# Performance work log

Hardware: AMD Instinct MI355X
Metric: run time of the kernel (lower is better)

The kernel has to match this reference:

```python
import jax, jax.numpy as jnp
import numpy as np

NUM_NODES = 100000
NUM_EDGES = 1600000
NUM_GRAPHS = 1000
NUM_REP = 16
R_DIM = 16
N_SCALARS = 16
N_CLASSES = 6
N_LAYERS = 3
L_MAX = 1
EPS = 1e-8


def get_rot(v):
    """2x2 SO(2) rotation from 2D vector angle, L_max=1. v:[n,2] -> [n,1,2,2]."""
    theta = jnp.arctan2(v[:, 1], v[:, 0])
    c, s = jnp.cos(theta), jnp.sin(theta)
    R = jnp.stack([jnp.stack([c, -s], -1), jnp.stack([s, c], -1)], -2)  # [n,2,2]
    return R[:, None]  # [n, L_max=1, 2, 2]


def bessel(d, number=R_DIM, end=1.0):
    """Bessel radial basis sqrt(2/end)*sin(n*pi*d/end)/d. d:[E] -> [E,number]."""
    n = jnp.arange(1, number + 1, dtype=d.dtype)
    d_safe = d[:, None] + EPS
    return jnp.sqrt(2.0 / end) * jnp.sin(n * jnp.pi * d[:, None] / end) / d_safe


def seg_sum(x, idx, n):
    return jax.ops.segment_sum(x, idx, num_segments=n)


def setup_inputs() -> dict:
    key = jax.random.key(0)
    ks = jax.random.split(key, 20)
    pos = jax.random.normal(ks[0], (NUM_NODES, 2), dtype=jnp.float32)
    edge_index = jax.random.randint(ks[1], (2, NUM_EDGES), 0, NUM_NODES)
    batch = jnp.sort(jax.random.randint(ks[2], (NUM_NODES,), 0, NUM_GRAPHS))
    s = 0.1
    return {
        "pos": pos,
        "W_emb_rot": s * jax.random.normal(ks[3], (NUM_REP, L_MAX, 2), jnp.float32),
        "w_s_emb": s * jax.random.normal(ks[4], (N_SCALARS,), jnp.float32),
        "b_s_emb": jnp.zeros((N_SCALARS,), jnp.float32),
        "Wg": s * jax.random.normal(ks[5], (N_LAYERS, R_DIM, NUM_REP), jnp.float32),
        "bg": jnp.zeros((N_LAYERS, NUM_REP), jnp.float32),
        "Wmix": s * jax.random.normal(ks[6], (N_LAYERS, NUM_REP, NUM_REP), jnp.float32),
        "Wgate": s * jax.random.normal(ks[7], (N_LAYERS, N_SCALARS, NUM_REP), jnp.float32),
        "bgate": jnp.zeros((N_LAYERS, NUM_REP), jnp.float32),
        "Ws1": s * jax.random.normal(ks[8], (N_LAYERS, N_SCALARS + R_DIM, N_SCALARS), jnp.float32),
        "bs1": jnp.zeros((N_LAYERS, N_SCALARS), jnp.float32),
        "W1": s * jax.random.normal(ks[9], (N_SCALARS + NUM_REP * L_MAX * 2, 3 * (N_SCALARS + NUM_REP * L_MAX * 2)), jnp.float32),
        "b1": jnp.zeros((3 * (N_SCALARS + NUM_REP * L_MAX * 2),), jnp.float32),
        "W2": s * jax.random.normal(ks[10], (3 * (N_SCALARS + NUM_REP * L_MAX * 2), N_CLASSES), jnp.float32),
        "b2": jnp.zeros((N_CLASSES,), jnp.float32),
        "edge_index": edge_index,
        "batch": batch,
    }


def reference(pos, W_emb_rot, w_s_emb, b_s_emb, Wg, bg, Wmix, Wgate, bgate,
              Ws1, bs1, W1, b1, W2, b2, edge_index, batch):
    N = pos.shape[0]
    # --- geometry under no_grad in torch ---
    posg = jax.lax.stop_gradient(pos)
    cnt = seg_sum(jnp.ones((N,), posg.dtype), batch, NUM_GRAPHS)
    mean = seg_sum(posg, batch, NUM_GRAPHS) / jnp.maximum(cnt, 1.0)[:, None]
    posg = posg - mean[batch]
    rot_theta = get_rot(posg)                        # [N,1,2,2]
    row, col = edge_index[0], edge_index[1]
    edge_vec = posg[row] - posg[col]                 # [E,2]
    rot = get_rot(edge_vec)                          # [E,1,2,2]
    dist = jnp.linalg.norm(edge_vec, axis=1)         # [E]

    dist_emb = bessel(dist)                          # [E,r_dim]

    # --- edge embedding -> node features ---
    e_rot = jnp.einsum('eklm,jkm->ejkl', rot, W_emb_rot)      # [E,rep,1,2]
    deg = jnp.maximum(seg_sum(jnp.ones((row.shape[0],), pos.dtype), row, N), 1.0)
    x_rot = seg_sum(e_rot, row, N) / deg[:, None, None, None]  # [N,rep,1,2]
    d_mean = seg_sum(dist, row, N) / deg
    x_s = jax.nn.leaky_relu(d_mean[:, None] * w_s_emb[None, :] + b_s_emb)  # [N,ns]

    rot_inv = jnp.swapaxes(rot, -1, -2)
    # --- EqBlocks: gather -> rotate-in -> radial mix -> rotate-out -> scatter ---
    for i in range(N_LAYERS):
        local = jnp.einsum('eklm,ejkm->ejkl', rot_inv, x_rot[col])   # [E,rep,1,2]
        g = dist_emb @ Wg[i] + bg[i]                                 # [E,rep]
        local = jnp.einsum('ij,ejkl->eikl', Wmix[i], local) * g[:, :, None, None]
        msg = jnp.einsum('eklm,ejkm->ejkl', rot, local)              # [E,rep,1,2]
        agg = seg_sum(msg, row, N) / deg[:, None, None, None]
        gate = jax.nn.sigmoid(x_s @ Wgate[i] + bgate[i])             # [N,rep]
        x_rot = x_rot + agg * gate[:, :, None, None]
        msg_s = jax.nn.leaky_relu(
            jnp.concatenate([x_s[col], dist_emb], axis=1) @ Ws1[i] + bs1[i])
        x_s = x_s + seg_sum(msg_s, row, N) / deg[:, None]

    # --- SO2OutU (faithful to given source) ---
    rot_theta_inv = jnp.swapaxes(rot_theta, -1, -2)                  # [N,1,2,2]
    x_out = jnp.einsum('njkm,nkml->njkl', x_rot, rot_theta_inv)      # [N,rep,1,2]
    x_cat = jnp.concatenate([x_s, x_out.reshape(N, -1)], axis=1)    # [N,48]
    u = jax.nn.leaky_relu(x_cat @ W1 + b1) @ W2 + b2                 # [N,n_classes]
    return seg_sum(u, batch, NUM_GRAPHS)                             # [G,n_classes]
```

## Files before the change

### kernel.cpp

```cpp
#include <hip/hip_runtime.h>
#include <hip/hip_fp16.h>
#include <math.h>

#define NREP 16
#define RDIM 16
#define NS   16
#define NC   6
#define H1   144
#define DBINS 64
#define TILE 4096
#define NBMAX 512
#define P2CAP 10240

static __device__ __forceinline__ float leaky(float v) { return v > 0.0f ? v : 0.01f * v; }

__global__ void __launch_bounds__(256) k_gsum_bhist(
    const float* __restrict__ pos, const int* __restrict__ batch, int N,
    float* __restrict__ gsum, float* __restrict__ gcnt,
    const int* __restrict__ ei, int E, int* __restrict__ bhist) {
  int t = threadIdx.x;
  __shared__ int h[NBMAX];
  for (int i = t; i < NBMAX; i += 256) h[i] = 0;
  __syncthreads();
  int base = blockIdx.x * TILE;
  int lim = min(base + TILE, E);
  for (int j = base + t; j < lim; j += 256) atomicAdd(&h[ei[j] >> 8], 1);
  __syncthreads();
  for (int i = t; i < NBMAX; i += 256)
    if (h[i] > 0) atomicAdd(&bhist[i], h[i]);

  __shared__ float bx[320], by[320], bc[320];
  int start = blockIdx.x * 256;
  if (start >= N) return;
  int n = start + t;
  int b0 = batch[min(start, N - 1)];
  int span = batch[min(start + 255, N - 1)] - b0;
  bool useLds = (span < 320);
  if (useLds) {
    for (int i = t; i <= span; i += 256) { bx[i] = 0.f; by[i] = 0.f; bc[i] = 0.f; }
    __syncthreads();
    if (n < N) {
      int rb = batch[n] - b0;
      atomicAdd(&bx[rb], pos[2 * n + 0]);
      atomicAdd(&by[rb], pos[2 * n + 1]);
      atomicAdd(&bc[rb], 1.0f);
    }
    __syncthreads();
    for (int i = t; i <= span; i += 256) {
      if (bc[i] != 0.0f) {
        atomicAdd(&gsum[2 * (b0 + i) + 0], bx[i]);
        atomicAdd(&gsum[2 * (b0 + i) + 1], by[i]);
        atomicAdd(&gcnt[b0 + i], bc[i]);
      }
    }
  } else if (n < N) {
    int b = batch[n];
    atomicAdd(&gsum[2 * b + 0], pos[2 * n + 0]);
    atomicAdd(&gsum[2 * b + 1], pos[2 * n + 1]);
    atomicAdd(&gcnt[b], 1.0f);
  }
}

__global__ void __launch_bounds__(256) k_center_bscan(
    const float* __restrict__ pos, const int* __restrict__ batch, int N, int E,
    const float* __restrict__ gsum, const float* __restrict__ gcnt,
    float* __restrict__ posc, float* __restrict__ cthn, float* __restrict__ sthn,
    const int* __restrict__ bhist, int* __restrict__ bbase, int* __restrict__ bcur, int NB) {
  int t = threadIdx.x;
  if (blockIdx.x == 0) {
    __shared__ int s[NBMAX];
    int v0 = (t < NB) ? bhist[t] : 0;
    int v1 = (t + 256 < NB) ? bhist[t + 256] : 0;
    s[t] = v0; s[t + 256] = v1;
    __syncthreads();
    for (int o = 1; o < NBMAX; o <<= 1) {
      int a0 = (t >= o) ? s[t - o] : 0;
      int a1 = s[t + 256 - o];
      __syncthreads();
      s[t] += a0; s[t + 256] += a1;
      __syncthreads();
    }
    if (t < NB)       { int ex = s[t] - v0;       bbase[t] = ex;       bcur[t] = ex; }
    if (t + 256 < NB) { int ex = s[t + 256] - v1; bbase[t + 256] = ex; bcur[t + 256] = ex; }
    if (t == 0) bbase[NB] = E;
  }
  int i = blockIdx.x * 256 + t;
  if (i < N) {
    int b = batch[i];
    float invc = 1.0f / fmaxf(gcnt[b], 1.0f);
    float px = pos[2 * i + 0] - gsum[2 * b + 0] * invc;
    float py = pos[2 * i + 1] - gsum[2 * b + 1] * invc;
    posc[2 * i + 0] = px;
    posc[2 * i + 1] = py;
    float r = sqrtf(px * px + py * py);
    if (r > 0.0f) { cthn[i] = px / r; sthn[i] = py / r; }
    else          { cthn[i] = 1.0f;  sthn[i] = 0.0f; }
  }
}

__global__ void __launch_bounds__(256) k_part1(
    const int* __restrict__ ei, int E,
    int* __restrict__ bcur, long long* __restrict__ ebuf) {
  __shared__ int hist[NBMAX], lofs[NBMAX], gbase[NBMAX], pc[NBMAX];
  __shared__ long long stg[TILE];
  __shared__ unsigned short bkt[TILE];
  int t = threadIdx.x;
  int base = blockIdx.x * TILE;
  int cntt = min(TILE, E - base);
  for (int i = t; i < NBMAX; i += 256) { hist[i] = 0; pc[i] = 0; }
  __syncthreads();
  int r[16], c[16];
#pragma unroll
  for (int i = 0; i < 16; i++) {
    int e = base + t + i * 256;
    r[i] = -1;
    if (e < E) {
      r[i] = ei[e];
      c[i] = ei[E + e];
      atomicAdd(&hist[r[i] >> 8], 1);
    }
  }
  __syncthreads();
  lofs[t] = hist[t]; lofs[t + 256] = hist[t + 256];
  __syncthreads();
  for (int o = 1; o < NBMAX; o <<= 1) {
    int a0 = (t >= o) ? lofs[t - o] : 0;
    int a1 = lofs[t + 256 - o];
    __syncthreads();
    lofs[t] += a0; lofs[t + 256] += a1;
    __syncthreads();
  }
  int e0 = lofs[t] - hist[t], e1 = lofs[t + 256] - hist[t + 256];
  __syncthreads();
  lofs[t] = e0; lofs[t + 256] = e1;
  __syncthreads();
  for (int i = t; i < NBMAX; i += 256)
    if (hist[i] > 0) gbase[i] = atomicAdd(&bcur[i], hist[i]);
  __syncthreads();
#pragma unroll
  for (int i = 0; i < 16; i++) {
    if (r[i] >= 0) {
      int b = r[i] >> 8;
      int l = lofs[b] + atomicAdd(&pc[b], 1);
      stg[l] = ((long long)r[i] << 32) | (unsigned int)c[i];
      bkt[l] = (unsigned short)b;
    }
  }
  __syncthreads();
  for (int j = t; j < cntt; j += 256) {
    int b = bkt[j];
    ebuf[gbase[b] + (j - lofs[b])] = stg[j];
  }
}

__global__ void __launch_bounds__(256) k_part2(
    const int* __restrict__ bbase, int N, int E,
    const long long* __restrict__ ebuf,
    int* __restrict__ off, int* __restrict__ cnt, int* __restrict__ dhist,
    int* __restrict__ adj) {
  __shared__ int lcnt[256], loff[256], lcur[256];
  __shared__ int lh[DBINS];
  __shared__ int ladj[P2CAP];
  int t = threadIdx.x;
  int b = blockIdx.x;
  int r0 = b << 8;
  int abeg = bbase[b];
  int aend = bbase[b + 1];
  int sz = aend - abeg;
  bool haveRow = (r0 + t < N);
  lcnt[t] = 0;
  if (t < DBINS) lh[t] = 0;
  __syncthreads();
  for (int j = abeg + t; j < aend; j += 256)
    atomicAdd(&lcnt[(int)(ebuf[j] >> 32) - r0], 1);
  __syncthreads();
  int v = lcnt[t];
  loff[t] = v;
  __syncthreads();
  for (int o = 1; o < 256; o <<= 1) {
    int u = (t >= o) ? loff[t - o] : 0;
    __syncthreads();
    loff[t] += u;
    __syncthreads();
  }
  int myoff = loff[t] - v;
  __syncthreads();
  loff[t] = myoff;
  lcur[t] = myoff;
  if (haveRow) {
    off[r0 + t] = abeg + myoff;
    cnt[r0 + t] = v;
    atomicAdd(&lh[min(v, DBINS - 1)], 1);
  }
  if (t == 0 && r0 + 256 >= N) off[N] = E;
  __syncthreads();
  if (t < DBINS && lh[t] > 0) atomicAdd(&dhist[t], lh[t]);
  if (sz <= P2CAP) {
    for (int j = abeg + t; j < aend; j += 256) {
      long long p = ebuf[j];
      int cl = (int)(unsigned int)(p & 0xffffffffLL);
      int rr = (int)(p >> 32) - r0;
      ladj[atomicAdd(&lcur[rr], 1)] = cl;
    }
    __syncthreads();
    for (int j = t; j < sz; j += 256) adj[abeg + j] = ladj[j];
  } else {
    for (int j = abeg + t; j < aend; j += 256) {
      long long p = ebuf[j];
      int cl = (int)(unsigned int)(p & 0xffffffffLL);
      int rr = (int)(p >> 32) - r0;
      adj[abeg + atomicAdd(&lcur[rr], 1)] = cl;
    }
  }
}

__global__ void __launch_bounds__(256) k_init16(
    int N, const int* __restrict__ off, const int* __restrict__ adj,
    const float* __restrict__ posc, float2* __restrict__ spc,
    const float* __restrict__ Wer, const float* __restrict__ wse, const float* __restrict__ bse,
    const float* __restrict__ Wmix, const float* __restrict__ Ws1, const float* __restrict__ bs1,
    const float* __restrict__ Wgate, const float* __restrict__ bgate,
    const int* __restrict__ cnt, const int* __restrict__ dhist,
    int* __restrict__ dcur, int* __restrict__ perm,
    float* __restrict__ xr, float* __restrict__ xs, uint2* __restrict__ yzg) {
  int t = threadIdx.x;
  int nchunk = (N + 255) >> 8;
  if ((int)blockIdx.x < nchunk) {
    __shared__ int sd[DBINS], lh[DBINS], base[DBINS];
    int dv = 0;
    if (t < DBINS) { dv = dhist[t]; sd[t] = dv; lh[t] = 0; }
    __syncthreads();
    for (int o = 1; o < DBINS; o <<= 1) {
      int u = (t >= o && t < DBINS) ? sd[t - o] : 0;
      __syncthreads();
      if (t < DBINS) sd[t] += u;
      __syncthreads();
    }
    int i = blockIdx.x * 256 + t;
    int b = 0, lr = 0;
    if (i < N) {
      b = min(cnt[i], DBINS - 1);
      lr = atomicAdd(&lh[b], 1);
    }
    __syncthreads();
    if (t < DBINS && lh[t] > 0) base[t] = (sd[t] - dv) + atomicAdd(&dcur[t], lh[t]);
    __syncthreads();
    if (i < N) perm[base[b] + lr] = i;
  }

  int idx = blockIdx.x * 256 + t;
  int n = idx >> 4, r = idx & 15;
  if (n >= N) return;
  int a = off[n], b = off[n + 1];
  float px = posc[2 * n + 0], py = posc[2 * n + 1];
  float C = 0.f, S = 0.f, D = 0.f;
  for (int k = a + r; k < b; k += 16) {
    int cl = adj[k];
    float dx = px - posc[2 * cl + 0];
    float dy = py - posc[2 * cl + 1];
    float d = sqrtf(dx * dx + dy * dy);
    float sp, cp;
    sincospif(d, &sp, &cp);
    float spp = 1.41421356237309515f * sp / (d + 1e-8f);
    spc[k] = make_float2(spp, 2.0f * cp);
    if (d > 0.0f) {
      float inv = 1.0f / d;
      C += dx * inv;
      S += dy * inv;
    } else {
      C += 1.0f;
    }
    D += d;
  }
#pragma unroll
  for (int o = 1; o < 16; o <<= 1) {
    C += __shfl_xor(C, o, 16);
    S += __shfl_xor(S, o, 16);
    D += __shfl_xor(D, o, 16);
  }
  float id = 1.0f / fmaxf((float)(b - a), 1.0f);
  C *= id; S *= id;
  float dm = D * id;
  float w0 = Wer[2 * r], w1 = Wer[2 * r + 1];
  float2 x;
  x.x = C * w0 - S * w1;
  x.y = S * w0 + C * w1;
  ((float2*)xr)[(size_t)n * 16 + r] = x;
  float s_new = leaky(dm * wse[r] + bse[r]);
  xs[(size_t)n * 16 + r] = s_new;

  float wmxn[16], wsan[16], wgtn[16];
#pragma unroll
  for (int q = 0; q < 16; q++) wmxn[q] = Wmix[r * 16 + q];
#pragma unroll
  for (int q = 0; q < 16; q++) wsan[q] = Ws1[q * 16 + r];
#pragma unroll
  for (int q = 0; q < 16; q++) wgtn[q] = Wgate[q * 16 + r];
  float y0 = 0.f, y1 = 0.f;
  float z = bs1[r], gtn = bgate[r];
#pragma unroll
  for (int j = 0; j < 16; j++) {
    float xj0 = __shfl(x.x, j, 16);
    float xj1 = __shfl(x.y, j, 16);
    float sj  = __shfl(s_new, j, 16);
    y0 += wmxn[j] * xj0;
    y1 += wmxn[j] * xj1;
    z  += wsan[j] * sj;
    gtn += wgtn[j] * sj;
  }
  gtn = 1.0f / (1.0f + __expf(-gtn));
  __half2 hA = __floats2half2_rn(y0, y1);
  __half2 hB = __floats2half2_rn(z, gtn);
  uint2 w2;
  w2.x = *(unsigned int*)&hA;
  w2.y = *(unsigned int*)&hB;
  yzg[(size_t)n * 16 + r] = w2;
}

__global__ void __launch_bounds__(256) k_layer(
    int N, const int* __restrict__ off,
    const int* __restrict__ adj, const float2* __restrict__ spc,
    const uint2* __restrict__ yzg, const int* __restrict__ perm,
    const float* __restrict__ Wg, const float* __restrict__ bg,
    const float* __restrict__ Ws1,
    float* xr, float* xs,
    int write_next, uint2* __restrict__ yzg_out,
    const float* __restrict__ Wmixn, const float* __restrict__ Ws1n,
    const float* __restrict__ bs1n,
    const float* __restrict__ Wgaten, const float* __restrict__ bgaten) {
  int idx = blockIdx.x * 256 + threadIdx.x;
  int g = idx >> 4, r = idx & 15;
  if (g >= N) return;
  int n = perm[g];
  float wg[16], ws[16];
#pragma unroll
  for (int q = 0; q < 16; q++) wg[q] = Wg[q * 16 + r];
#pragma unroll
  for (int q = 0; q < 16; q++) ws[q] = Ws1[(16 + q) * 16 + r];
  float bgr = bg[r];

  int a = off[n], bnd = off[n + 1];
  float acc0 = 0.f, acc1 = 0.f, accs = 0.f;
  if (a < bnd) {
    int last = bnd - 1;
    int    c0 = adj[a];               float2 p0 = spc[a];
    int    c1 = adj[min(a + 1, last)]; float2 p1 = spc[min(a + 1, last)];
    int    cn = adj[min(a + 2, last)]; float2 p2 = spc[min(a + 2, last)];
    uint2 Y0 = yzg[(c0 << 4) + r];
    uint2 Y1 = yzg[(c1 << 4) + r];
    int k = a;
    for (; k + 3 < bnd; k++) {
      int c3 = adj[k + 3];
      float2 p3 = spc[k + 3];
      uint2 Y2 = yzg[(cn << 4) + r];
      float skm1 = 0.f, sk = p0.x, c2 = p0.y;
      float g1 = bgr, dot = 0.f;
#pragma unroll
      for (int q = 0; q < RDIM; q++) {
        g1  = __builtin_fmaf(sk, wg[q], g1);
        dot = __builtin_fmaf(sk, ws[q], dot);
        float sn = __builtin_fmaf(c2, sk, -skm1);
        skm1 = sk; sk = sn;
      }
      float2 f01 = __half22float2(*(__half2*)&Y0.x);
      float2 fzg = __half22float2(*(__half2*)&Y0.y);
      acc0 = __builtin_fmaf(g1, f01.x, acc0);
      acc1 = __builtin_fmaf(g1, f01.y, acc1);
      accs += leaky(dot + fzg.x);
      c0 = c1; p0 = p1; c1 = cn; p1 = p2; cn = c3; p2 = p3; Y0 = Y1; Y1 = Y2;
    }
    for (; k < bnd; k++) {
      uint2 Y2 = Y1;
      if (k + 2 < bnd) Y2 = yzg[(cn << 4) + r];
      float skm1 = 0.f, sk = p0.x, c2 = p0.y;
      float g1 = bgr, dot = 0.f;
#pragma unroll
      for (int q = 0; q < RDIM; q++) {
        g1  = __builtin_fmaf(sk, wg[q], g1);
        dot = __builtin_fmaf(sk, ws[q], dot);
        float sn = __builtin_fmaf(c2, sk, -skm1);
        skm1 = sk; sk = sn;
      }
      float2 f01 = __half22float2(*(__half2*)&Y0.x);
      float2 fzg = __half22float2(*(__half2*)&Y0.y);
      acc0 = __builtin_fmaf(g1, f01.x, acc0);
      acc1 = __builtin_fmaf(g1, f01.y, acc1);
      accs += leaky(dot + fzg.x);
      c0 = c1; p0 = p1; c1 = cn; p1 = p2; Y0 = Y1; Y1 = Y2;
    }
  }
  float id = 1.0f / fmaxf((float)(bnd - a), 1.0f);
  uint2 Yg = yzg[(n << 4) + r];
  float gt = __half22float2(*(__half2*)&Yg.y).y;
  float2* xr2 = (float2*)xr;
  float2 x = xr2[(n << 4) + r];
  x.x += acc0 * id * gt;
  x.y += acc1 * id * gt;
  xr2[(n << 4) + r] = x;
  float s_new = xs[(n << 4) + r] + accs * id;
  xs[(n << 4) + r] = s_new;

  if (write_next) {
    float wmxn[16], wsan[16], wgtn[16];
#pragma unroll
    for (int q = 0; q < 16; q++) wmxn[q] = Wmixn[r * 16 + q];
#pragma unroll
    for (int q = 0; q < 16; q++) wsan[q] = Ws1n[q * 16 + r];
#pragma unroll
    for (int q = 0; q < 16; q++) wgtn[q] = Wgaten[q * 16 + r];
    float y0 = 0.f, y1 = 0.f;
    float z = bs1n[r], gtn = bgaten[r];
#pragma unroll
    for (int j = 0; j < 16; j++) {
      float xj0 = __shfl(x.x, j, 16);
      float xj1 = __shfl(x.y, j, 16);
      float sj  = __shfl(s_new, j, 16);
      y0 += wmxn[j] * xj0;
      y1 += wmxn[j] * xj1;
      z  += wsan[j] * sj;
      gtn += wgtn[j] * sj;
    }
    gtn = 1.0f / (1.0f + __expf(-gtn));
    __half2 hA = __floats2half2_rn(y0, y1);
    __half2 hB = __floats2half2_rn(z, gtn);
    uint2 w2;
    w2.x = *(unsigned int*)&hA;
    w2.y = *(unsigned int*)&hB;
    yzg_out[(n << 4) + r] = w2;
  }
}

__global__ void __launch_bounds__(128) k_final(
    int N, const float* __restrict__ xr, const float* __restrict__ xs,
    const float* __restrict__ cthn, const float* __restrict__ sthn,
    const int* __restrict__ batch,
    const float* __restrict__ W1, const float* __restrict__ b1,
    const float* __restrict__ W2, const float* __restrict__ b2,
    float* __restrict__ out) {
  __shared__ float obin[320 * 6];
  int t = threadIdx.x;
  int start = blockIdx.x * 128;
  int n = start + t;
  int b0 = batch[min(start, N - 1)];
  int span = batch[min(start + 127, N - 1)] - b0;
  bool useLds = (span < 320);
  if (useLds) for (int i = t; i < (span + 1) * 6; i += 128) obin[i] = 0.f;
  __syncthreads();

  float u[NC];
  bool act = (n < N);
  if (act) {
    float xc[48];
    const float4* xs4 = (const float4*)(xs + (size_t)n * NS);
#pragma unroll
    for (int j = 0; j < 4; j++) {
      float4 v = xs4[j];
      xc[4 * j + 0] = v.x; xc[4 * j + 1] = v.y; xc[4 * j + 2] = v.z; xc[4 * j + 3] = v.w;
    }
    float c = cthn[n], s = sthn[n];
    const float4* xr4 = (const float4*)(xr + (size_t)n * 32);
#pragma unroll
    for (int j = 0; j < 8; j++) {
      float4 v = xr4[j];
      xc[16 + 4 * j + 0] = c * v.x - s * v.y;
      xc[16 + 4 * j + 1] = s * v.x + c * v.y;
      xc[16 + 4 * j + 2] = c * v.z - s * v.w;
      xc[16 + 4 * j + 3] = s * v.z + c * v.w;
    }
#pragma unroll
    for (int q = 0; q < NC; q++) u[q] = b2[q];
    for (int h = 0; h < H1; h += 4) {
      float a0 = b1[h + 0], a1 = b1[h + 1], a2 = b1[h + 2], a3 = b1[h + 3];
#pragma unroll
      for (int q = 0; q < 48; q++) {
        float4 w = *(const float4*)(W1 + (size_t)q * H1 + h);
        float x = xc[q];
        a0 = __builtin_fmaf(x, w.x, a0);
        a1 = __builtin_fmaf(x, w.y, a1);
        a2 = __builtin_fmaf(x, w.z, a2);
        a3 = __builtin_fmaf(x, w.w, a3);
      }
      a0 = leaky(a0); a1 = leaky(a1); a2 = leaky(a2); a3 = leaky(a3);
#pragma unroll
      for (int q = 0; q < NC; q++)
        u[q] += a0 * W2[(h + 0) * 6 + q] + a1 * W2[(h + 1) * 6 + q]
              + a2 * W2[(h + 2) * 6 + q] + a3 * W2[(h + 3) * 6 + q];
    }
  }
  if (useLds) {
    if (act) {
      int rb = batch[n] - b0;
#pragma unroll
      for (int q = 0; q < NC; q++) atomicAdd(&obin[rb * 6 + q], u[q]);
    }
    __syncthreads();
    for (int i = t; i < (span + 1) * 6; i += 128) atomicAdd(&out[b0 * 6 + i], obin[i]);
  } else if (act) {
    int b = batch[n];
#pragma unroll
    for (int q = 0; q < NC; q++) atomicAdd(&out[b * 6 + q], u[q]);
  }
}

extern "C" void kernel_launch(void* const* d_in, const int* in_sizes, int n_in,
                              void* d_out, int out_size, void* d_ws, size_t ws_size,
                              hipStream_t stream) {
  const float* pos   = (const float*)d_in[0];
  const float* Wer   = (const float*)d_in[1];
  const float* wse   = (const float*)d_in[2];
  const float* bse   = (const float*)d_in[3];
  const float* Wg    = (const float*)d_in[4];
  const float* bg    = (const float*)d_in[5];
  const float* Wmix  = (const float*)d_in[6];
  const float* Wgate = (const float*)d_in[7];
  const float* bgate = (const float*)d_in[8];
  const float* Ws1   = (const float*)d_in[9];
  const float* bs1   = (const float*)d_in[10];
  const float* W1    = (const float*)d_in[11];
  const float* b1    = (const float*)d_in[12];
  const float* W2    = (const float*)d_in[13];
  const float* b2    = (const float*)d_in[14];
  const int*   ei    = (const int*)d_in[15];
  const int*   batch = (const int*)d_in[16];
  float* out = (float*)d_out;

  int N = in_sizes[0] / 2;
  int E = in_sizes[15] / 2;
  int G = out_size / NC;
  int NB = (N + 255) / 256;

  float* W = (float*)d_ws;
  size_t o = 0;
  float* gsum   = W + o; o += (size_t)2 * G;
  float* gcnt   = W + o; o += (size_t)G;
  int*   bhist  = (int*)(W + o); o += (size_t)NBMAX;
  int*   dhist  = (int*)(W + o); o += (size_t)DBINS;
  int*   dcur   = (int*)(W + o); o += (size_t)DBINS;
  size_t zero_bytes = o * 4;
  o = (o + 3) & ~(size_t)3;
  float* posc   = W + o; o += (size_t)2 * N;
  float* cthn   = W + o; o += (size_t)N;
  float* sthn   = W + o; o += (size_t)N;
  int*   off    = (int*)(W + o); o += (size_t)N + 1; o = (o + 3) & ~(size_t)3;
  int*   bbase  = (int*)(W + o); o += (size_t)NBMAX + 1;
  int*   bcur   = (int*)(W + o); o += (size_t)NBMAX;
  int*   cnt    = (int*)(W + o); o += (size_t)N;
  int*   perm   = (int*)(W + o); o += (size_t)N; o = (o + 3) & ~(size_t)3;
  int*   adj    = (int*)(W + o); o += (size_t)E; o = (o + 1) & ~(size_t)1;
  float2* spc   = (float2*)(W + o); o += (size_t)2 * E;
  long long* ebuf = (long long*)spc;
  uint2* yzgA   = (uint2*)(W + o); o += (size_t)32 * N;
  uint2* yzgB   = (uint2*)(W + o); o += (size_t)32 * N;
  float* xr     = W + o; o += (size_t)N * 32;
  float* xs     = W + o; o += (size_t)N * 16;
  (void)ws_size;

  hipMemsetAsync(d_ws, 0, zero_bytes, stream);
  hipMemsetAsync(d_out, 0, (size_t)out_size * 4, stream);

  int nbN  = (N + 255) / 256;
  int nbT  = (E + TILE - 1) / TILE;
  int nbG  = nbT > nbN ? nbT : nbN;
  int nbN16 = ((size_t)N * 16 + 255) / 256;
  int nbF  = (N + 127) / 128;

  k_gsum_bhist<<<nbG, 256, 0, stream>>>(pos, batch, N, gsum, gcnt, ei, E, bhist);
  k_center_bscan<<<nbN, 256, 0, stream>>>(pos, batch, N, E, gsum, gcnt,
                                          posc, cthn, sthn, bhist, bbase, bcur, NB);
  k_part1<<<nbT, 256, 0, stream>>>(ei, E, bcur, ebuf);
  k_part2<<<NB, 256, 0, stream>>>(bbase, N, E, ebuf, off, cnt, dhist, adj);
  k_init16<<<nbN16, 256, 0, stream>>>(N, off, adj, posc, spc, Wer, wse, bse,
                                      Wmix, Ws1, bs1, Wgate, bgate,
                                      cnt, dhist, dcur, perm,
                                      xr, xs, yzgA);

  k_layer<<<nbN16, 256, 0, stream>>>(N, off, adj, spc, yzgA, perm,
                                     Wg, bg, Ws1, xr, xs,
                                     1, yzgB,
                                     Wmix + 256, Ws1 + 512, bs1 + 16, Wgate + 256, bgate + 16);
  k_layer<<<nbN16, 256, 0, stream>>>(N, off, adj, spc, yzgB, perm,
                                     Wg + 256, bg + 16, Ws1 + 512, xr, xs,
                                     1, yzgA,
                                     Wmix + 512, Ws1 + 1024, bs1 + 32, Wgate + 512, bgate + 32);
  k_layer<<<nbN16, 256, 0, stream>>>(N, off, adj, spc, yzgA, perm,
                                     Wg + 512, bg + 32, Ws1 + 1024, xr, xs,
                                     0, yzgB,
                                     Wmix, Ws1, bs1, Wgate, bgate);

  k_final<<<nbF, 128, 0, stream>>>(N, xr, xs, cthn, sthn, batch, W1, b1, W2, b2, out);
}
```

Baseline: 409.9 us.

## Pair each 16-lane group with two nodes from opposite ends of degree order

Each 16-lane group in the layer kernel now handles two nodes, perm[g] and perm[N-1-g], taken from opposite ends of the degree-sorted permutation. Both edge loops are interleaved in one loop, and the grid is halved. The aim is to even out per-group edge counts so wavefronts carry less imbalance, and to expose more independent gather loads per thread. In exchange it costs more registers, divergent branches inside the loop, and less thread-level parallelism.

Measured after the change: 481.0 us. +17.3%, slower.

```diff
diff --git a/kernel.cpp b/kernel.cpp
--- a/kernel.cpp
+++ b/kernel.cpp
@@ -330,8 +330,13 @@
     const float* __restrict__ Wgaten, const float* __restrict__ bgaten) {
   int idx = blockIdx.x * 256 + threadIdx.x;
   int g = idx >> 4, r = idx & 15;
-  if (g >= N) return;
-  int n = perm[g];
+  int Hh = (N + 1) >> 1;
+  if (g >= Hh) return;
+  int nA = perm[g];
+  int gB = N - 1 - g;
+  bool hasB = gB > g;
+  int nB = perm[gB];
+
   float wg[16], ws[16];
 #pragma unroll
   for (int q = 0; q < 16; q++) wg[q] = Wg[q * 16 + r];
@@ -339,66 +344,96 @@
   for (int q = 0; q < 16; q++) ws[q] = Ws1[(16 + q) * 16 + r];
   float bgr = bg[r];
 
-  int a = off[n], bnd = off[n + 1];
-  float acc0 = 0.f, acc1 = 0.f, accs = 0.f;
-  if (a < bnd) {
-    int last = bnd - 1;
-    int    c0 = adj[a];               float2 p0 = spc[a];
-    int    c1 = adj[min(a + 1, last)]; float2 p1 = spc[min(a + 1, last)];
-    int    cn = adj[min(a + 2, last)]; float2 p2 = spc[min(a + 2, last)];
-    uint2 Y0 = yzg[(c0 << 4) + r];
-    uint2 Y1 = yzg[(c1 << 4) + r];
-    int k = a;
-    for (; k + 3 < bnd; k++) {
-      int c3 = adj[k + 3];
-      float2 p3 = spc[k + 3];
-      uint2 Y2 = yzg[(cn << 4) + r];
-      float skm1 = 0.f, sk = p0.x, c2 = p0.y;
-      float g1 = bgr, dot = 0.f;
-#pragma unroll
-      for (int q = 0; q < RDIM; q++) {
-        g1  = __builtin_fmaf(sk, wg[q], g1);
-        dot = __builtin_fmaf(sk, ws[q], dot);
-        float sn = __builtin_fmaf(c2, sk, -skm1);
-        skm1 = sk; sk = sn;
-      }
-      float2 f01 = __half22float2(*(__half2*)&Y0.x);
-      float2 fzg = __half22float2(*(__half2*)&Y0.y);
-      acc0 = __builtin_fmaf(g1, f01.x, acc0);
-      acc1 = __builtin_fmaf(g1, f01.y, acc1);
-      accs += leaky(dot + fzg.x);
-      c0 = c1; p0 = p1; c1 = cn; p1 = p2; cn = c3; p2 = p3; Y0 = Y1; Y1 = Y2;
-    }
-    for (; k < bnd; k++) {
-      uint2 Y2 = Y1;
-      if (k + 2 < bnd) Y2 = yzg[(cn << 4) + r];
-      float skm1 = 0.f, sk = p0.x, c2 = p0.y;
-      float g1 = bgr, dot = 0.f;
-#pragma unroll
-      for (int q = 0; q < RDIM; q++) {
-        g1  = __builtin_fmaf(sk, wg[q], g1);
-        dot = __builtin_fmaf(sk, ws[q], dot);
-        float sn = __builtin_fmaf(c2, sk, -skm1);
-        skm1 = sk; sk = sn;
-      }
-      float2 f01 = __half22float2(*(__half2*)&Y0.x);
-      float2 fzg = __half22float2(*(__half2*)&Y0.y);
-      acc0 = __builtin_fmaf(g1, f01.x, acc0);
-      acc1 = __builtin_fmaf(g1, f01.y, acc1);
-      accs += leaky(dot + fzg.x);
-      c0 = c1; p0 = p1; c1 = cn; p1 = p2; Y0 = Y1; Y1 = Y2;
-    }
-  }
-  float id = 1.0f / fmaxf((float)(bnd - a), 1.0f);
-  uint2 Yg = yzg[(n << 4) + r];
-  float gt = __half22float2(*(__half2*)&Yg.y).y;
+  int aA = off[nA], bndA = off[nA + 1];
+  int aB = 0, bndB = 0;
+  if (hasB) { aB = off[nB]; bndB = off[nB + 1]; }
+  int mA = bndA - aA, mB = bndB - aB;
+  int lastA = bndA - 1, lastB = bndB - 1;
+
+  float accA0 = 0.f, accA1 = 0.f, accAs = 0.f;
+  float accB0 = 0.f, accB1 = 0.f, accBs = 0.f;
+  float2 pA0, pA1, pB0, pB1;
+  uint2 YA0, YA1, YB0, YB1;
+  if (mA > 0) {
+    int i1 = min(aA + 1, lastA);
+    int c0 = adj[aA], c1 = adj[i1];
+    pA0 = spc[aA]; pA1 = spc[i1];
+    YA0 = yzg[(c0 << 4) + r]; YA1 = yzg[(c1 << 4) + r];
+  }
+  if (mB > 0) {
+    int i1 = min(aB + 1, lastB);
+    int c0 = adj[aB], c1 = adj[i1];
+    pB0 = spc[aB]; pB1 = spc[i1];
+    YB0 = yzg[(c0 << 4) + r]; YB1 = yzg[(c1 << 4) + r];
+  }
+
+#define EDGE_BODY(P0, Y0, A0, A1, AS)                                          \
+  {                                                                            \
+    float skm1 = 0.f, sk = (P0).x, cc = (P0).y;                                \
+    float g1 = bgr, dot = 0.f;                                                 \
+    _Pragma("unroll")                                                          \
+    for (int q = 0; q < RDIM; q++) {                                           \
+      g1  = __builtin_fmaf(sk, wg[q], g1);                                     \
+      dot = __builtin_fmaf(sk, ws[q], dot);                                    \
+      float sn = __builtin_fmaf(cc, sk, -skm1);                                \
+      skm1 = sk; sk = sn;                                                      \
+    }                                                                          \
+    float2 f01 = __half22float2(*(__half2*)&(Y0).x);                           \
+    float2 fzg = __half22float2(*(__half2*)&(Y0).y);                           \
+    A0 = __builtin_fmaf(g1, f01.x, A0);                                        \
+    A1 = __builtin_fmaf(g1, f01.y, A1);                                        \
+    AS += leaky(dot + fzg.x);                                                  \
+  }
+
+  int m = mA > mB ? mA : mB;
+  for (int s = 0; s < m; s++) {
+    bool doA = s < mA, doB = s < mB;
+    float2 pA2, pB2; uint2 YA2, YB2;
+    if (doA) {
+      int i2 = min(aA + s + 2, lastA);
+      int c2 = adj[i2];
+      pA2 = spc[i2]; YA2 = yzg[(c2 << 4) + r];
+    }
+    if (doB) {
+      int i2 = min(aB + s + 2, lastB);
+      int c2 = adj[i2];
+      pB2 = spc[i2]; YB2 = yzg[(c2 << 4) + r];
+    }
+    if (doA) {
+      EDGE_BODY(pA0, YA0, accA0, accA1, accAs);
+      pA0 = pA1; YA0 = YA1; pA1 = pA2; YA1 = YA2;
+    }
+    if (doB) {
+      EDGE_BODY(pB0, YB0, accB0, accB1, accBs);
+      pB0 = pB1; YB0 = YB1; pB1 = pB2; YB1 = YB2;
+    }
+  }
+#undef EDGE_BODY
+
   float2* xr2 = (float2*)xr;
-  float2 x = xr2[(n << 4) + r];
-  x.x += acc0 * id * gt;
-  x.y += acc1 * id * gt;
-  xr2[(n << 4) + r] = x;
-  float s_new = xs[(n << 4) + r] + accs * id;
-  xs[(n << 4) + r] = s_new;
+  float idA = 1.0f / fmaxf((float)mA, 1.0f);
+  uint2 YgA = yzg[(nA << 4) + r];
+  float gtA = __half22float2(*(__half2*)&YgA.y).y;
+  float2 xA = xr2[(nA << 4) + r];
+  xA.x += accA0 * idA * gtA;
+  xA.y += accA1 * idA * gtA;
+  xr2[(nA << 4) + r] = xA;
+  float sA = xs[(nA << 4) + r] + accAs * idA;
+  xs[(nA << 4) + r] = sA;
+
+  float2 xB = make_float2(0.f, 0.f);
+  float sB = 0.f;
+  if (hasB) {
+    float idB = 1.0f / fmaxf((float)mB, 1.0f);
+    uint2 YgB = yzg[(nB << 4) + r];
+    float gtB = __half22float2(*(__half2*)&YgB.y).y;
+    xB = xr2[(nB << 4) + r];
+    xB.x += accB0 * idB * gtB;
+    xB.y += accB1 * idB * gtB;
+    xr2[(nB << 4) + r] = xB;
+    sB = xs[(nB << 4) + r] + accBs * idB;
+    xs[(nB << 4) + r] = sB;
+  }
 
   if (write_next) {
     float wmxn[16], wsan[16], wgtn[16];
@@ -408,25 +443,33 @@
     for (int q = 0; q < 16; q++) wsan[q] = Ws1n[q * 16 + r];
 #pragma unroll
     for (int q = 0; q < 16; q++) wgtn[q] = Wgaten[q * 16 + r];
-    float y0 = 0.f, y1 = 0.f;
-    float z = bs1n[r], gtn = bgaten[r];
-#pragma unroll
-    for (int j = 0; j < 16; j++) {
-      float xj0 = __shfl(x.x, j, 16);
-      float xj1 = __shfl(x.y, j, 16);
-      float sj  = __shfl(s_new, j, 16);
-      y0 += wmxn[j] * xj0;
-      y1 += wmxn[j] * xj1;
-      z  += wsan[j] * sj;
-      gtn += wgtn[j] * sj;
-    }
-    gtn = 1.0f / (1.0f + __expf(-gtn));
-    __half2 hA = __floats2half2_rn(y0, y1);
-    __half2 hB = __floats2half2_rn(z, gtn);
-    uint2 w2;
-    w2.x = *(unsigned int*)&hA;
-    w2.y = *(unsigned int*)&hB;
-    yzg_out[(n << 4) + r] = w2;
+
+#define PRE_STORE(XV, SV, NODE)                                                \
+    {                                                                          \
+      float y0 = 0.f, y1 = 0.f;                                                \
+      float z = bs1n[r], gtn = bgaten[r];                                      \
+      _Pragma("unroll")                                                        \
+      for (int j = 0; j < 16; j++) {                                           \
+        float xj0 = __shfl((XV).x, j, 16);                                     \
+        float xj1 = __shfl((XV).y, j, 16);                                     \
+        float sj  = __shfl((SV), j, 16);                                       \
+        y0 += wmxn[j] * xj0;                                                   \
+        y1 += wmxn[j] * xj1;                                                   \
+        z  += wsan[j] * sj;                                                    \
+        gtn += wgtn[j] * sj;                                                   \
+      }                                                                        \
+      gtn = 1.0f / (1.0f + __expf(-gtn));                                      \
+      __half2 hA_ = __floats2half2_rn(y0, y1);                                 \
+      __half2 hB_ = __floats2half2_rn(z, gtn);                                 \
+      uint2 w2;                                                                \
+      w2.x = *(unsigned int*)&hA_;                                             \
+      w2.y = *(unsigned int*)&hB_;                                             \
+      yzg_out[((NODE) << 4) + r] = w2;                                         \
+    }
+
+    PRE_STORE(xA, sA, nA);
+    if (hasB) PRE_STORE(xB, sB, nB);
+#undef PRE_STORE
   }
 }
 
@@ -528,6 +571,7 @@
   int E = in_sizes[15] / 2;
   int G = out_size / NC;
   int NB = (N + 255) / 256;
+  int Hh = (N + 1) / 2;
 
   float* W = (float*)d_ws;
   size_t o = 0;
@@ -562,6 +606,7 @@
   int nbT  = (E + TILE - 1) / TILE;
   int nbG  = nbT > nbN ? nbT : nbN;
   int nbN16 = ((size_t)N * 16 + 255) / 256;
+  int nbL  = ((size_t)Hh * 16 + 255) / 256;
   int nbF  = (N + 127) / 128;
 
   k_gsum_bhist<<<nbG, 256, 0, stream>>>(pos, batch, N, gsum, gcnt, ei, E, bhist);
@@ -574,18 +619,18 @@
                                       cnt, dhist, dcur, perm,
                                       xr, xs, yzgA);
 
-  k_layer<<<nbN16, 256, 0, stream>>>(N, off, adj, spc, yzgA, perm,
-                                     Wg, bg, Ws1, xr, xs,
-                                     1, yzgB,
-                                     Wmix + 256, Ws1 + 512, bs1 + 16, Wgate + 256, bgate + 16);
-  k_layer<<<nbN16, 256, 0, stream>>>(N, off, adj, spc, yzgB, perm,
-                                     Wg + 256, bg + 16, Ws1 + 512, xr, xs,
-                                     1, yzgA,
-                                     Wmix + 512, Ws1 + 1024, bs1 + 32, Wgate + 512, bgate + 32);
-  k_layer<<<nbN16, 256, 0, stream>>>(N, off, adj, spc, yzgA, perm,
-                                     Wg + 512, bg + 32, Ws1 + 1024, xr, xs,
-                                     0, yzgB,
-                                     Wmix, Ws1, bs1, Wgate, bgate);
+  k_layer<<<nbL, 256, 0, stream>>>(N, off, adj, spc, yzgA, perm,
+                                   Wg, bg, Ws1, xr, xs,
+                                   1, yzgB,
+                                   Wmix + 256, Ws1 + 512, bs1 + 16, Wgate + 256, bgate + 16);
+  k_layer<<<nbL, 256, 0, stream>>>(N, off, adj, spc, yzgB, perm,
+                                   Wg + 256, bg + 16, Ws1 + 512, xr, xs,
+                                   1, yzgA,
+                                   Wmix + 512, Ws1 + 1024, bs1 + 32, Wgate + 512, bgate + 32);
+  k_layer<<<nbL, 256, 0, stream>>>(N, off, adj, spc, yzgA, perm,
+                                   Wg + 512, bg + 32, Ws1 + 1024, xr, xs,
+                                   0, yzgB,
+                                   Wmix, Ws1, bs1, Wgate, bgate);
 
   k_final<<<nbF, 128, 0, stream>>>(N, xr, xs, cthn, sthn, batch, W1, b1, W2, b2, out);
 }
```
